# Optimization experiments

Hardware: AMD Instinct MI355X
Metric: run time of the kernel (lower is better)

The kernel has to match this reference:

```python
import jax, jax.numpy as jnp
import numpy as np

B, N, E = 8, 2048, 1024


def setup_inputs() -> dict:
    key = jax.random.key(0)
    x = jax.random.normal(key, (B, N, E), dtype=jnp.float32)
    pos = jnp.ones((N - 1,), dtype=jnp.float32)
    zero = jnp.ones((1,), dtype=jnp.float32)
    neg = jnp.ones((N - 1,), dtype=jnp.float32)
    return {"x": x, "pos": pos, "zero": zero, "neg": neg}


def reference(x, pos, zero, neg):
    # x: [b, n, e]; Toeplitz matvec via circular FFT convolution of length 2n.
    b, n, e = x.shape
    # circulant kernel: [zero, pos[:n-1], zero, neg[-(n-1):]] -> length 2n
    a = jnp.concatenate([zero, pos[: n - 1], zero, neg[-(n - 1):]])
    # torch: fft(x, 2n, dim=1, norm='ortho')
    y = jnp.fft.fft(x, n=2 * n, axis=1, norm="ortho")  # [b, 2n, e] complex
    # torch: fft(a) with default ('backward') norm, i.e. unnormalized forward
    v = jnp.fft.fft(a)[None, :, None]                   # [1, 2n, 1]
    u = v * y
    out = jnp.fft.ifft(u, n=2 * n, axis=1, norm="ortho")[:, :n, :].real
    return out.astype(x.dtype)
```

## Files before the change

### kernel.cpp

```cpp
#include <hip/hip_runtime.h>
#include <stdint.h>


#define B_ 8
#define N_ 2048
#define NF 4096
#define E_ 1024

#define BUFSZ (NF + (NF >> 5))
__device__ __forceinline__ int P(int n) { return n + (n >> 5); }
#define PERM(r) ((((r) & 3) << 2) | ((r) >> 2))

__device__ __forceinline__ unsigned short f32_to_bf16_rne(float f) {
    union { float f; unsigned int u; } cv; cv.f = f;
    unsigned int u = cv.u;
    u += 0x7fffu + ((u >> 16) & 1u);
    return (unsigned short)(u >> 16);
}
__device__ __forceinline__ float bf16_to_f32(unsigned short u) {
    union { unsigned int u; float f; } cv; cv.u = ((unsigned int)u) << 16; return cv.f;
}
__device__ __forceinline__ void cmul(float& ar, float& ai, float br, float bi) {
    float t = ar * br - ai * bi; ai = ar * bi + ai * br; ar = t;
}
__device__ __forceinline__ void cmulc(float& ar, float& ai, float br, float bi) {
    float t = ar * br + ai * bi; ai = ai * br - ar * bi; ar = t;
}

__device__ __forceinline__ void dft4(float& x0r, float& x0i, float& x1r, float& x1i,
                                     float& x2r, float& x2i, float& x3r, float& x3i,
                                     float sg) {
    float t0r = x0r + x2r, t0i = x0i + x2i;
    float t1r = x0r - x2r, t1i = x0i - x2i;
    float t2r = x1r + x3r, t2i = x1i + x3i;
    float t3r = x1r - x3r, t3i = x1i - x3i;
    x0r = t0r + t2r; x0i = t0i + t2i;
    x2r = t0r - t2r; x2i = t0i - t2i;
    x1r = t1r - sg * t3i; x1i = t1i + sg * t3r;
    x3r = t1r + sg * t3i; x3i = t1i - sg * t3r;
}

template<int SG>
__device__ __forceinline__ void dft16_layer1(float* xr, float* xi) {
    const float sg = (float)SG;
#pragma unroll
    for (int n0 = 0; n0 < 4; ++n0)
        dft4(xr[n0], xi[n0], xr[n0 + 4], xi[n0 + 4],
             xr[n0 + 8], xi[n0 + 8], xr[n0 + 12], xi[n0 + 12], sg);
}
template<int SG>
__device__ __forceinline__ void dft16_layer1_pad(float* xr, float* xi) {
    const float sg = (float)SG;
#pragma unroll
    for (int n0 = 0; n0 < 4; ++n0) {
        float ar = xr[n0], ai = xi[n0], br = xr[n0 + 4], bi = xi[n0 + 4];
        xr[n0]      = ar + br;       xi[n0]      = ai + bi;
        xr[n0 + 4]  = ar - sg * bi;  xi[n0 + 4]  = ai + sg * br;
        xr[n0 + 8]  = ar - br;       xi[n0 + 8]  = ai - bi;
        xr[n0 + 12] = ar + sg * bi;  xi[n0 + 12] = ai - sg * br;
    }
}
template<int SG>
__device__ __forceinline__ void dft16_twiddle(float* xr, float* xi) {
    const float sg = (float)SG;
    const float C1 = 0.923879532511286756f;
    const float S1 = 0.382683432365089772f;
    const float H  = 0.707106781186547524f;
    cmul(xr[5],  xi[5],  C1,  sg * S1);
    cmul(xr[9],  xi[9],  H,   sg * H);
    cmul(xr[13], xi[13], S1,  sg * C1);
    cmul(xr[6],  xi[6],  H,   sg * H);
    cmul(xr[10], xi[10], 0.f, sg);
    cmul(xr[14], xi[14], -H,  sg * H);
    cmul(xr[7],  xi[7],  S1,  sg * C1);
    cmul(xr[11], xi[11], -H,  sg * H);
    cmul(xr[15], xi[15], -C1, -sg * S1);
}
template<int SG>
__device__ __forceinline__ void dft16_layer2(float* xr, float* xi) {
    const float sg = (float)SG;
#pragma unroll
    for (int k1 = 0; k1 < 4; ++k1)
        dft4(xr[4 * k1], xi[4 * k1], xr[4 * k1 + 1], xi[4 * k1 + 1],
             xr[4 * k1 + 2], xi[4 * k1 + 2], xr[4 * k1 + 3], xi[4 * k1 + 3], sg);
}
template<int SG>
__device__ __forceinline__ void dft16(float* xr, float* xi) {
    dft16_layer1<SG>(xr, xi);
    dft16_twiddle<SG>(xr, xi);
    dft16_layer2<SG>(xr, xi);
}

template<int INV, int L>
__device__ __forceinline__ void fft_stage(float2* buf, const float2* __restrict__ tw2, int t) {
    constexpr int Lq = L / 16;
    int g = t / Lq;
    int j = t - g * Lq;
    int base = g * L + j;
    float xr[16], xi[16];
#pragma unroll
    for (int r = 0; r < 16; ++r) {
        float2 v = buf[P(base + r * Lq)];
        xr[r] = v.x; xi[r] = v.y;
    }
    float2 w1 = tw2[j * (NF / L)];
    float w1r = w1.x, w1i = INV ? -w1.y : w1.y;
    if (INV) {
        float wr = 1.f, wi = 0.f;
#pragma unroll
        for (int r = 1; r < 16; ++r) { cmul(wr, wi, w1r, w1i); cmul(xr[r], xi[r], wr, wi); }
        dft16<1>(xr, xi);
#pragma unroll
        for (int r = 0; r < 16; ++r) {
            float2 v; v.x = xr[PERM(r)]; v.y = xi[PERM(r)];
            buf[P(base + r * Lq)] = v;
        }
    } else {
        dft16<-1>(xr, xi);
        { float2 v; v.x = xr[0]; v.y = xi[0]; buf[P(base)] = v; }
        float wr = 1.f, wi = 0.f;
#pragma unroll
        for (int r = 1; r < 16; ++r) {
            cmul(wr, wi, w1r, w1i);
            float yr = xr[PERM(r)], yi = xi[PERM(r)];
            cmul(yr, yi, wr, wi);
            float2 v; v.x = yr; v.y = yi;
            buf[P(base + r * Lq)] = v;
        }
    }
}

__global__ __launch_bounds__(256) void build_tw(float2* tw2, float2* tw4096, float2* tw256) {
    const float TPI = -6.28318530717958647692f;
    int blk = blockIdx.x, t = threadIdx.x;
    if (blk < 16) {
        int k = blk * 256 + t;
        float s, c;
        __sincosf(TPI * (float)k * (1.f / 4096.f), &s, &c);
        float2 v; v.x = c; v.y = s;
        tw2[k] = v;
        int rj = (blk * t) & (NF - 1);
        __sincosf(TPI * (float)rj * (1.f / 4096.f), &s, &c);
        float2 w; w.x = c; w.y = s;
        tw4096[blk * 256 + t] = w;
    } else {
        int r = t >> 4, j = t & 15;
        float s, c;
        __sincosf(TPI * (float)(r * j) * (1.f / 256.f), &s, &c);
        float2 v; v.x = c; v.y = s;
        tw256[t] = v;
    }
}

__global__ __launch_bounds__(256) void build_V(const float* __restrict__ pos,
                                               const float* __restrict__ zero,
                                               const float* __restrict__ neg,
                                               const float2* __restrict__ tw2,
                                               float2* __restrict__ V2) {
    __shared__ float2 buf[BUFSZ];
    int t = threadIdx.x;
#pragma unroll
    for (int it = 0; it < 16; ++it) {
        int n = t + 256 * it;
        float v;
        if (n == 0) v = zero[0];
        else if (n < N_) v = pos[n - 1];
        else if (n == N_) v = zero[0];
        else v = neg[n - (N_ + 1)];
        float2 c; c.x = v; c.y = 0.f;
        buf[P(n)] = c;
    }
    __syncthreads();
    fft_stage<0, 4096>(buf, tw2, t); __syncthreads();
    fft_stage<0, 256>(buf, tw2, t);  __syncthreads();
    fft_stage<0, 16>(buf, tw2, t);   __syncthreads();
    const float s = 1.f / (float)NF;
#pragma unroll
    for (int it = 0; it < 16; ++it) {
        int n = t + 256 * it;
        float2 c = buf[P(n)];
        c.x *= s; c.y *= s;
        V2[n] = c;
    }
}

__global__ __launch_bounds__(256) void transpose_x(const float* __restrict__ x,
                                                   unsigned short* __restrict__ xT) {
    __shared__ float tile[64][66];
    int b  = blockIdx.z;
    int j0 = blockIdx.y * 64;
    int e0 = blockIdx.x * 64;
    int t  = threadIdx.x;

    int e4 = t & 15, jr = t >> 4;
#pragma unroll
    for (int it = 0; it < 4; ++it) {
        int j = jr + it * 16;
        const float4 v = *(const float4*)(x + ((size_t)(b * N_ + j0 + j) * E_) + e0 + e4 * 4);
        tile[e4 * 4 + 0][j] = v.x;
        tile[e4 * 4 + 1][j] = v.y;
        tile[e4 * 4 + 2][j] = v.z;
        tile[e4 * 4 + 3][j] = v.w;
    }
    __syncthreads();
    int j2 = (t & 31) * 2, er = t >> 5;
#pragma unroll
    for (int it = 0; it < 8; ++it) {
        int e = er + it * 8;
        float2 v = *(const float2*)&tile[e][j2];
        union { unsigned short s[2]; unsigned int u; } pk;
        pk.s[0] = f32_to_bf16_rne(v.x);
        pk.s[1] = f32_to_bf16_rne(v.y);
        *(unsigned int*)(xT + ((size_t)(b * E_ + e0 + e)) * N_ + j0 + j2) = pk.u;
    }
}

__global__ __launch_bounds__(256) void fft_conv(const unsigned short* __restrict__ xT,
                                                const float2* __restrict__ tw4096,
                                                const float2* __restrict__ tw256,
                                                const float2* __restrict__ V2,
                                                float* __restrict__ out) {
    __shared__ float2 buf[BUFSZ];
    int t = threadIdx.x;
    int bid = blockIdx.x;
    int xcd = bid & 7;
    int q = bid >> 3;
    int b = q >> 6;
    int e0 = (xcd * 64 + (q & 63)) * 2;

    const unsigned short* r0 = xT + ((size_t)(b * E_ + e0)) * N_;
    const unsigned short* r1 = r0 + N_;

    float xr[16], xi[16];

#pragma unroll
    for (int r = 0; r < 8; ++r) {
        int n = t + 256 * r;
        xr[r] = bf16_to_f32(r0[n]);
        xi[r] = bf16_to_f32(r1[n]);
    }
#pragma unroll
    for (int r = 8; r < 16; ++r) { xr[r] = 0.f; xi[r] = 0.f; }
    dft16_layer1_pad<-1>(xr, xi);
    dft16_twiddle<-1>(xr, xi);
    dft16_layer2<-1>(xr, xi);
    { float2 v; v.x = xr[0]; v.y = xi[0]; buf[P(t)] = v; }
#pragma unroll
    for (int r = 1; r < 16; ++r) {
        float2 w = tw4096[r * 256 + t];
        float yr = xr[PERM(r)], yi = xi[PERM(r)];
        cmul(yr, yi, w.x, w.y);
        float2 v; v.x = yr; v.y = yi;
        buf[P(t + 256 * r)] = v;
    }
    __syncthreads();

    int g = t >> 4, j = t & 15;
    int base = g * 256 + j;
#pragma unroll
    for (int r = 0; r < 16; ++r) {
        float2 v = buf[P(base + 16 * r)];
        xr[r] = v.x; xi[r] = v.y;
    }
    dft16<-1>(xr, xi);
    { float2 v; v.x = xr[0]; v.y = xi[0]; buf[P(base)] = v; }
#pragma unroll
    for (int r = 1; r < 16; ++r) {
        float2 w = tw256[r * 16 + j];
        float yr = xr[PERM(r)], yi = xi[PERM(r)];
        cmul(yr, yi, w.x, w.y);
        float2 v; v.x = yr; v.y = yi;
        buf[P(base + 16 * r)] = v;
    }
    __syncthreads();

    {
        int mb = 16 * t;
#pragma unroll
        for (int r = 0; r < 16; ++r) {
            float2 v = buf[P(mb + r)];
            xr[r] = v.x; xi[r] = v.y;
        }
        dft16<-1>(xr, xi);
        float yr2[16], yi2[16];
        const float4* Vv = (const float4*)(V2 + mb);
#pragma unroll
        for (int h = 0; h < 8; ++h) {
            float4 vv = Vv[h];
            int r = 2 * h;
            float ar = xr[PERM(r)], ai = xi[PERM(r)];
            yr2[r] = ar * vv.x - ai * vv.y;
            yi2[r] = ar * vv.y + ai * vv.x;
            r = 2 * h + 1;
            ar = xr[PERM(r)]; ai = xi[PERM(r)];
            yr2[r] = ar * vv.z - ai * vv.w;
            yi2[r] = ar * vv.w + ai * vv.z;
        }
        dft16<1>(yr2, yi2);
#pragma unroll
        for (int r = 0; r < 16; ++r) {
            float2 v; v.x = yr2[PERM(r)]; v.y = yi2[PERM(r)];
            buf[P(mb + r)] = v;
        }
    }
    __syncthreads();

#pragma unroll
    for (int r = 0; r < 16; ++r) {
        float2 v = buf[P(base + 16 * r)];
        xr[r] = v.x; xi[r] = v.y;
    }
#pragma unroll
    for (int r = 1; r < 16; ++r) {
        float2 w = tw256[r * 16 + j];
        cmulc(xr[r], xi[r], w.x, w.y);
    }
    dft16<1>(xr, xi);
#pragma unroll
    for (int r = 0; r < 16; ++r) {
        float2 v; v.x = xr[PERM(r)]; v.y = xi[PERM(r)];
        buf[P(base + 16 * r)] = v;
    }
    __syncthreads();

#pragma unroll
    for (int r = 0; r < 16; ++r) {
        float2 v = buf[P(t + 256 * r)];
        xr[r] = v.x; xi[r] = v.y;
    }
#pragma unroll
    for (int r = 1; r < 16; ++r) {
        float2 w = tw4096[r * 256 + t];
        cmulc(xr[r], xi[r], w.x, w.y);
    }
    dft16_layer1<1>(xr, xi);
    dft16_twiddle<1>(xr, xi);
    float* ob = out + ((size_t)b * N_) * E_ + e0;
#pragma unroll
    for (int k1 = 0; k1 < 4; ++k1) {
        float a0r = xr[4 * k1],     a0i = xi[4 * k1];
        float a1r = xr[4 * k1 + 1], a1i = xi[4 * k1 + 1];
        float a2r = xr[4 * k1 + 2], a2i = xi[4 * k1 + 2];
        float a3r = xr[4 * k1 + 3], a3i = xi[4 * k1 + 3];
        float t0r = a0r + a2r, t0i = a0i + a2i;
        float t1r = a0r - a2r, t1i = a0i - a2i;
        float t2r = a1r + a3r, t2i = a1i + a3i;
        float t3r = a1r - a3r, t3i = a1i - a3i;
        float2 v0; v0.x = t0r + t2r; v0.y = t0i + t2i;
        float2 v1; v1.x = t1r - t3i; v1.y = t1i + t3r;
        *(float2*)(ob + (size_t)(t + 256 * k1) * E_)       = v0;
        *(float2*)(ob + (size_t)(t + 256 * (k1 + 4)) * E_) = v1;
    }
}

__global__ __launch_bounds__(256) void naive_toep(const float* __restrict__ x,
                                                  const float* __restrict__ pos,
                                                  const float* __restrict__ zero,
                                                  const float* __restrict__ neg,
                                                  float* __restrict__ out) {
    int bid = blockIdx.x;
    int e   = (bid & 3) * 256 + threadIdx.x;
    int k   = (bid >> 2) & (N_ - 1);
    int b   = bid >> 13;
    float zv = zero[0];
    float acc = 0.f;
    const float* xb = x + (size_t)b * N_ * E_ + e;
    for (int jj = 0; jj < N_; ++jj) {
        float c = (jj < k) ? pos[k - jj - 1] : (jj == k) ? zv : neg[N_ - 1 - jj + k];
        acc += c * xb[(size_t)jj * E_];
    }
    out[((size_t)(b * N_ + k)) * E_ + e] = acc;
}

extern "C" void kernel_launch(void* const* d_in, const int* in_sizes, int n_in,
                              void* d_out, int out_size, void* d_ws, size_t ws_size,
                              hipStream_t stream) {
    const float* x    = (const float*)d_in[0];
    const float* pos  = (const float*)d_in[1];
    const float* zero = (const float*)d_in[2];
    const float* neg  = (const float*)d_in[3];
    float* out = (float*)d_out;

    const size_t needX = (size_t)B_ * E_ * N_ * sizeof(unsigned short);
    const size_t need  = needX + (3 * (size_t)NF + 256) * sizeof(float2);
    if (ws_size >= need) {
        unsigned short* xT = (unsigned short*)d_ws;
        float2* tw2    = (float2*)((char*)d_ws + needX);
        float2* V2     = tw2 + NF;
        float2* tw4096 = V2 + NF;
        float2* tw256  = tw4096 + NF;
        build_tw<<<17, 256, 0, stream>>>(tw2, tw4096, tw256);
        transpose_x<<<dim3(16, 32, 8), 256, 0, stream>>>(x, xT);
        build_V<<<1, 256, 0, stream>>>(pos, zero, neg, tw2, V2);
        fft_conv<<<4096, 256, 0, stream>>>(xT, tw4096, tw256, V2, out);
    } else {
        naive_toep<<<65536, 256, 0, stream>>>(x, pos, zero, neg, out);
    }
}
```

Baseline: 205.9 us.

## Drop transpose pass; read x directly in FFT kernel and merge table builds

Removes the separate transpose-to-bf16 kernel and has fft_conv read two adjacent columns of x straight from the original layout as float2 loads strided by E. The twiddle and kernel-spectrum setup kernels are merged into one launch that computes twiddles with sincos instead of a table. LDS padding is replaced with an XOR swizzle so the buffer shrinks, and launch bounds now request 5 blocks per CU. The goal is to skip a full read/write of the input and cut launch count. The trade-off is that the strided 8-byte global reads coalesce poorly.

```diff
diff --git a/kernel.cpp b/kernel.cpp
--- a/kernel.cpp
+++ b/kernel.cpp
@@ -7,19 +7,9 @@
 #define NF 4096
 #define E_ 1024
 
-#define BUFSZ (NF + (NF >> 5))
-__device__ __forceinline__ int P(int n) { return n + (n >> 5); }
+__device__ __forceinline__ int P(int n) { return n ^ ((n >> 4) & 15) ^ ((n >> 8) & 15); }
 #define PERM(r) ((((r) & 3) << 2) | ((r) >> 2))
 
-__device__ __forceinline__ unsigned short f32_to_bf16_rne(float f) {
-    union { float f; unsigned int u; } cv; cv.f = f;
-    unsigned int u = cv.u;
-    u += 0x7fffu + ((u >> 16) & 1u);
-    return (unsigned short)(u >> 16);
-}
-__device__ __forceinline__ float bf16_to_f32(unsigned short u) {
-    union { unsigned int u; float f; } cv; cv.u = ((unsigned int)u) << 16; return cv.f;
-}
 __device__ __forceinline__ void cmul(float& ar, float& ai, float br, float bi) {
     float t = ar * br - ai * bi; ai = ar * bi + ai * br; ar = t;
 }
@@ -91,136 +81,85 @@
     dft16_layer2<SG>(xr, xi);
 }
 
-template<int INV, int L>
-__device__ __forceinline__ void fft_stage(float2* buf, const float2* __restrict__ tw2, int t) {
+template<int L>
+__device__ __forceinline__ void fwd_stage_sincos(float2* buf, int t) {
     constexpr int Lq = L / 16;
     int g = t / Lq;
     int j = t - g * Lq;
     int base = g * L + j;
+    const float TPI = -6.28318530717958647692f;
     float xr[16], xi[16];
 #pragma unroll
     for (int r = 0; r < 16; ++r) {
         float2 v = buf[P(base + r * Lq)];
         xr[r] = v.x; xi[r] = v.y;
     }
-    float2 w1 = tw2[j * (NF / L)];
-    float w1r = w1.x, w1i = INV ? -w1.y : w1.y;
-    if (INV) {
-        float wr = 1.f, wi = 0.f;
-#pragma unroll
-        for (int r = 1; r < 16; ++r) { cmul(wr, wi, w1r, w1i); cmul(xr[r], xi[r], wr, wi); }
-        dft16<1>(xr, xi);
-#pragma unroll
-        for (int r = 0; r < 16; ++r) {
-            float2 v; v.x = xr[PERM(r)]; v.y = xi[PERM(r)];
-            buf[P(base + r * Lq)] = v;
-        }
-    } else {
-        dft16<-1>(xr, xi);
-        { float2 v; v.x = xr[0]; v.y = xi[0]; buf[P(base)] = v; }
-        float wr = 1.f, wi = 0.f;
-#pragma unroll
-        for (int r = 1; r < 16; ++r) {
-            cmul(wr, wi, w1r, w1i);
-            float yr = xr[PERM(r)], yi = xi[PERM(r)];
-            cmul(yr, yi, wr, wi);
-            float2 v; v.x = yr; v.y = yi;
-            buf[P(base + r * Lq)] = v;
-        }
-    }
-}
-
-__global__ __launch_bounds__(256) void build_tw(float2* tw2, float2* tw4096, float2* tw256) {
+    dft16<-1>(xr, xi);
+    { float2 v; v.x = xr[0]; v.y = xi[0]; buf[P(base)] = v; }
+#pragma unroll
+    for (int r = 1; r < 16; ++r) {
+        float s, c;
+        __sincosf(TPI * (float)(j * r) * (1.f / (float)L), &s, &c);
+        float yr = xr[PERM(r)], yi = xi[PERM(r)];
+        cmul(yr, yi, c, s);
+        float2 v; v.x = yr; v.y = yi;
+        buf[P(base + r * Lq)] = v;
+    }
+}
+
+__global__ __launch_bounds__(256) void build_tables(const float* __restrict__ pos,
+                                                    const float* __restrict__ zero,
+                                                    const float* __restrict__ neg,
+                                                    float2* __restrict__ tw4096,
+                                                    float2* __restrict__ tw256,
+                                                    float2* __restrict__ V2) {
+    __shared__ float2 buf[NF];
     const float TPI = -6.28318530717958647692f;
     int blk = blockIdx.x, t = threadIdx.x;
     if (blk < 16) {
-        int k = blk * 256 + t;
         float s, c;
-        __sincosf(TPI * (float)k * (1.f / 4096.f), &s, &c);
+        __sincosf(TPI * (float)(blk * t) * (1.f / 4096.f), &s, &c);
         float2 v; v.x = c; v.y = s;
-        tw2[k] = v;
-        int rj = (blk * t) & (NF - 1);
-        __sincosf(TPI * (float)rj * (1.f / 4096.f), &s, &c);
-        float2 w; w.x = c; w.y = s;
-        tw4096[blk * 256 + t] = w;
-    } else {
+        tw4096[blk * 256 + t] = v;
+    } else if (blk == 16) {
         int r = t >> 4, j = t & 15;
         float s, c;
         __sincosf(TPI * (float)(r * j) * (1.f / 256.f), &s, &c);
         float2 v; v.x = c; v.y = s;
         tw256[t] = v;
-    }
-}
-
-__global__ __launch_bounds__(256) void build_V(const float* __restrict__ pos,
-                                               const float* __restrict__ zero,
-                                               const float* __restrict__ neg,
-                                               const float2* __restrict__ tw2,
-                                               float2* __restrict__ V2) {
-    __shared__ float2 buf[BUFSZ];
-    int t = threadIdx.x;
-#pragma unroll
-    for (int it = 0; it < 16; ++it) {
-        int n = t + 256 * it;
-        float v;
-        if (n == 0) v = zero[0];
-        else if (n < N_) v = pos[n - 1];
-        else if (n == N_) v = zero[0];
-        else v = neg[n - (N_ + 1)];
-        float2 c; c.x = v; c.y = 0.f;
-        buf[P(n)] = c;
-    }
-    __syncthreads();
-    fft_stage<0, 4096>(buf, tw2, t); __syncthreads();
-    fft_stage<0, 256>(buf, tw2, t);  __syncthreads();
-    fft_stage<0, 16>(buf, tw2, t);   __syncthreads();
-    const float s = 1.f / (float)NF;
-#pragma unroll
-    for (int it = 0; it < 16; ++it) {
-        int n = t + 256 * it;
-        float2 c = buf[P(n)];
-        c.x *= s; c.y *= s;
-        V2[n] = c;
-    }
-}
-
-__global__ __launch_bounds__(256) void transpose_x(const float* __restrict__ x,
-                                                   unsigned short* __restrict__ xT) {
-    __shared__ float tile[64][66];
-    int b  = blockIdx.z;
-    int j0 = blockIdx.y * 64;
-    int e0 = blockIdx.x * 64;
-    int t  = threadIdx.x;
-
-    int e4 = t & 15, jr = t >> 4;
-#pragma unroll
-    for (int it = 0; it < 4; ++it) {
-        int j = jr + it * 16;
-        const float4 v = *(const float4*)(x + ((size_t)(b * N_ + j0 + j) * E_) + e0 + e4 * 4);
-        tile[e4 * 4 + 0][j] = v.x;
-        tile[e4 * 4 + 1][j] = v.y;
-        tile[e4 * 4 + 2][j] = v.z;
-        tile[e4 * 4 + 3][j] = v.w;
-    }
-    __syncthreads();
-    int j2 = (t & 31) * 2, er = t >> 5;
-#pragma unroll
-    for (int it = 0; it < 8; ++it) {
-        int e = er + it * 8;
-        float2 v = *(const float2*)&tile[e][j2];
-        union { unsigned short s[2]; unsigned int u; } pk;
-        pk.s[0] = f32_to_bf16_rne(v.x);
-        pk.s[1] = f32_to_bf16_rne(v.y);
-        *(unsigned int*)(xT + ((size_t)(b * E_ + e0 + e)) * N_ + j0 + j2) = pk.u;
-    }
-}
-
-__global__ __launch_bounds__(256) void fft_conv(const unsigned short* __restrict__ xT,
-                                                const float2* __restrict__ tw4096,
-                                                const float2* __restrict__ tw256,
-                                                const float2* __restrict__ V2,
-                                                float* __restrict__ out) {
-    __shared__ float2 buf[BUFSZ];
+    } else {
+#pragma unroll
+        for (int it = 0; it < 16; ++it) {
+            int n = t + 256 * it;
+            float v;
+            if (n == 0) v = zero[0];
+            else if (n < N_) v = pos[n - 1];
+            else if (n == N_) v = zero[0];
+            else v = neg[n - (N_ + 1)];
+            float2 cc; cc.x = v; cc.y = 0.f;
+            buf[P(n)] = cc;
+        }
+        __syncthreads();
+        fwd_stage_sincos<4096>(buf, t); __syncthreads();
+        fwd_stage_sincos<256>(buf, t);  __syncthreads();
+        fwd_stage_sincos<16>(buf, t);   __syncthreads();
+        const float s = 1.f / (float)NF;
+#pragma unroll
+        for (int it = 0; it < 16; ++it) {
+            int n = t + 256 * it;
+            float2 c = buf[P(n)];
+            c.x *= s; c.y *= s;
+            V2[n] = c;
+        }
+    }
+}
+
+__global__ __launch_bounds__(256, 5) void fft_conv(const float* __restrict__ x,
+                                                   const float2* __restrict__ tw4096,
+                                                   const float2* __restrict__ tw256,
+                                                   const float2* __restrict__ V2,
+                                                   float* __restrict__ out) {
+    __shared__ float2 buf[NF];
     int t = threadIdx.x;
     int bid = blockIdx.x;
     int xcd = bid & 7;
@@ -228,16 +167,14 @@
     int b = q >> 6;
     int e0 = (xcd * 64 + (q & 63)) * 2;
 
-    const unsigned short* r0 = xT + ((size_t)(b * E_ + e0)) * N_;
-    const unsigned short* r1 = r0 + N_;
+    const float* xb = x + ((size_t)b * N_) * E_ + e0;
 
     float xr[16], xi[16];
 
 #pragma unroll
     for (int r = 0; r < 8; ++r) {
-        int n = t + 256 * r;
-        xr[r] = bf16_to_f32(r0[n]);
-        xi[r] = bf16_to_f32(r1[n]);
+        float2 v = *(const float2*)(xb + (size_t)(t + 256 * r) * E_);
+        xr[r] = v.x; xi[r] = v.y;
     }
 #pragma unroll
     for (int r = 8; r < 16; ++r) { xr[r] = 0.f; xi[r] = 0.f; }
@@ -381,18 +318,13 @@
     const float* neg  = (const float*)d_in[3];
     float* out = (float*)d_out;
 
-    const size_t needX = (size_t)B_ * E_ * N_ * sizeof(unsigned short);
-    const size_t need  = needX + (3 * (size_t)NF + 256) * sizeof(float2);
+    const size_t need = (2 * (size_t)NF + 256) * sizeof(float2);
     if (ws_size >= need) {
-        unsigned short* xT = (unsigned short*)d_ws;
-        float2* tw2    = (float2*)((char*)d_ws + needX);
-        float2* V2     = tw2 + NF;
-        float2* tw4096 = V2 + NF;
+        float2* tw4096 = (float2*)d_ws;
         float2* tw256  = tw4096 + NF;
-        build_tw<<<17, 256, 0, stream>>>(tw2, tw4096, tw256);
-        transpose_x<<<dim3(16, 32, 8), 256, 0, stream>>>(x, xT);
-        build_V<<<1, 256, 0, stream>>>(pos, zero, neg, tw2, V2);
-        fft_conv<<<4096, 256, 0, stream>>>(xT, tw4096, tw256, V2, out);
+        float2* V2     = tw256 + 256;
+        build_tables<<<18, 256, 0, stream>>>(pos, zero, neg, tw4096, tw256, V2);
+        fft_conv<<<4096, 256, 0, stream>>>(x, tw4096, tw256, V2, out);
     } else {
         naive_toep<<<65536, 256, 0, stream>>>(x, pos, zero, neg, out);
     }
```

Measured after the change: 327.6 us. +59.1%, slower.
